# Performance work log

Hardware: AMD Instinct MI355X
Metric: run time of the kernel (lower is better)

The kernel has to match this reference:

```python
import jax, jax.numpy as jnp
import numpy as np

EPS = 1e-8  # numerical guard in padded (masked) softmax denominator


def setup_inputs() -> dict:
    key = jax.random.key(0)
    k1, k2 = jax.random.split(key)
    B, N, D = 8, 2048, 3
    coordinates = jax.random.normal(k1, (B, N, D), dtype=jnp.float32)
    masks = (jax.random.uniform(k2, (B, N, N)) < 0.9).astype(jnp.float32)
    sigma = jnp.ones((1,), dtype=jnp.float32)  # NonNeg learned scalar
    return {"coordinates": coordinates, "masks": masks, "sigma": sigma}


def reference(coordinates, masks, sigma):
    # pairwise squared euclidean distances: ||xi||^2 - 2 xi.xj + ||xj||^2
    norms = jnp.sum(coordinates ** 2, axis=-1, keepdims=True)            # [B,N,1]
    inner = jnp.einsum('bnd,bmd->bnm', coordinates, coordinates)         # [B,N,N]
    distances = norms - 2.0 * inner + jnp.swapaxes(norms, -1, -2)        # [B,N,N]
    # Gaussian kernel
    A = jnp.exp(-distances / (sigma ** 2))                               # [B,N,N]
    # padded_softmax: mask then row-normalize (A is positive, so this is a
    # masked softmax over -d/sigma^2 along the last axis)
    A = A * masks
    return A / (jnp.sum(A, axis=-1, keepdims=True) + EPS)
```

## Files before the change

### kernel.cpp

```cpp
#include <hip/hip_runtime.h>
#include <math.h>


#define NN      2048
#define THREADS 256
#define WPB     4
#define EPS     1e-8f

typedef float vfloat4 __attribute__((ext_vector_type(4)));

__global__ __launch_bounds__(THREADS) void gauss_adj_kernel(
    const float* __restrict__ coords,
    const float* __restrict__ masks,
    const float* __restrict__ sigma,
    float* __restrict__ out)
{
    const int row  = blockIdx.x * WPB + (threadIdx.x >> 6);
    const int lane = threadIdx.x & 63;
    const int b    = row >> 11;
    const int i    = row & (NN - 1);

    const float* cb = coords + (size_t)b * NN * 3;
    const float xi = cb[i * 3 + 0];
    const float yi = cb[i * 3 + 1];
    const float zi = cb[i * 3 + 2];
    const float s  = sigma[0];
    const float inv_s2 = 1.0f / (s * s);

    const vfloat4* mrow = (const vfloat4*)(masks + (size_t)row * NN);
    vfloat4*       orow = (vfloat4*)(out + (size_t)row * NN);
    const float4*  c4   = (const float4*)cb;

    vfloat4 a[8];
    float lsum = 0.0f;

    #pragma unroll
    for (int w = 0; w < 8; ++w) {
        const int q = w * 64 + lane;
        const vfloat4 m = __builtin_nontemporal_load(&mrow[q]);
        const float4 c0 = c4[3 * q + 0];
        const float4 c1 = c4[3 * q + 1];
        const float4 c2 = c4[3 * q + 2];

        float dx, dy, dz, d;
        dx = xi - c0.x; dy = yi - c0.y; dz = zi - c0.z;
        d  = dx * dx + dy * dy + dz * dz;
        const float a0 = __expf(-d * inv_s2) * m.x;

        dx = xi - c0.w; dy = yi - c1.x; dz = zi - c1.y;
        d  = dx * dx + dy * dy + dz * dz;
        const float a1 = __expf(-d * inv_s2) * m.y;

        dx = xi - c1.z; dy = yi - c1.w; dz = zi - c2.x;
        d  = dx * dx + dy * dy + dz * dz;
        const float a2 = __expf(-d * inv_s2) * m.z;

        dx = xi - c2.y; dy = yi - c2.z; dz = zi - c2.w;
        d  = dx * dx + dy * dy + dz * dz;
        const float a3 = __expf(-d * inv_s2) * m.w;

        vfloat4 av;
        av.x = a0; av.y = a1; av.z = a2; av.w = a3;
        a[w] = av;
        lsum += (a0 + a1) + (a2 + a3);
    }

    #pragma unroll
    for (int off = 32; off > 0; off >>= 1)
        lsum += __shfl_xor(lsum, off, 64);

    const float inv = 1.0f / (lsum + EPS);

    #pragma unroll
    for (int w = 0; w < 8; ++w) {
        const int q = w * 64 + lane;
        vfloat4 o = a[w];
        o.x *= inv; o.y *= inv; o.z *= inv; o.w *= inv;
        __builtin_nontemporal_store(o, &orow[q]);
    }
}

extern "C" void kernel_launch(void* const* d_in, const int* in_sizes, int n_in,
                              void* d_out, int out_size, void* d_ws, size_t ws_size,
                              hipStream_t stream) {
    const float* coords = (const float*)d_in[0];
    const float* masks  = (const float*)d_in[1];
    const float* sigma  = (const float*)d_in[2];
    float* out = (float*)d_out;

    const int B    = in_sizes[0] / (NN * 3);
    const int rows = B * NN;
    gauss_adj_kernel<<<rows / WPB, THREADS, 0, stream>>>(coords, masks, sigma, out);
}
```

Before: 237.2 us.

## Process four rows per wave with double-buffered mask loads and LDS coordinates

```diff
diff --git a/kernel.cpp b/kernel.cpp
--- a/kernel.cpp
+++ b/kernel.cpp
@@ -4,80 +4,94 @@
 
 #define NN      2048
 #define THREADS 256
-#define WPB     4
+#define RPW     4
+#define ROWS_PER_BLOCK 16
 #define EPS     1e-8f
 
-typedef float vfloat4 __attribute__((ext_vector_type(4)));
+typedef float vf4 __attribute__((ext_vector_type(4)));
 
-__global__ __launch_bounds__(THREADS) void gauss_adj_kernel(
+__global__ __launch_bounds__(THREADS, 4) void gauss_adj_kernel(
     const float* __restrict__ coords,
     const float* __restrict__ masks,
     const float* __restrict__ sigma,
     float* __restrict__ out)
 {
-    const int row  = blockIdx.x * WPB + (threadIdx.x >> 6);
-    const int lane = threadIdx.x & 63;
-    const int b    = row >> 11;
-    const int i    = row & (NN - 1);
+    const int tid  = threadIdx.x;
+    const int wid  = tid >> 6;
+    const int lane = tid & 63;
+    const int rowBase = blockIdx.x * ROWS_PER_BLOCK;
+    const int b = rowBase >> 11;
+
+    __shared__ __align__(16) float sx[NN];
+    __shared__ __align__(16) float sy[NN];
+    __shared__ __align__(16) float sz[NN];
 
     const float* cb = coords + (size_t)b * NN * 3;
-    const float xi = cb[i * 3 + 0];
-    const float yi = cb[i * 3 + 1];
-    const float zi = cb[i * 3 + 2];
-    const float s  = sigma[0];
-    const float inv_s2 = 1.0f / (s * s);
+    for (int idx = tid; idx < NN; idx += THREADS) {
+        sx[idx] = cb[idx * 3 + 0];
+        sy[idx] = cb[idx * 3 + 1];
+        sz[idx] = cb[idx * 3 + 2];
+    }
+    __syncthreads();
 
-    const vfloat4* mrow = (const vfloat4*)(masks + (size_t)row * NN);
-    vfloat4*       orow = (vfloat4*)(out + (size_t)row * NN);
-    const float4*  c4   = (const float4*)cb;
+    const float s = sigma[0];
+    const float cexp = -1.44269504088896341f / (s * s);
 
-    vfloat4 a[8];
-    float lsum = 0.0f;
+    const int r0 = rowBase + wid * RPW;
+    const vf4* sx4 = (const vf4*)sx;
+    const vf4* sy4 = (const vf4*)sy;
+    const vf4* sz4 = (const vf4*)sz;
 
-    #pragma unroll
-    for (int w = 0; w < 8; ++w) {
-        const int q = w * 64 + lane;
-        const vfloat4 m = __builtin_nontemporal_load(&mrow[q]);
-        const float4 c0 = c4[3 * q + 0];
-        const float4 c1 = c4[3 * q + 1];
-        const float4 c2 = c4[3 * q + 2];
+    vf4 A[8], B[8];
 
-        float dx, dy, dz, d;
-        dx = xi - c0.x; dy = yi - c0.y; dz = zi - c0.z;
-        d  = dx * dx + dy * dy + dz * dz;
-        const float a0 = __expf(-d * inv_s2) * m.x;
+#define LOADM(BUF, R) { \
+    const vf4* mrow_ = (const vf4*)(masks + (size_t)(r0 + (R)) * NN); \
+    _Pragma("unroll") \
+    for (int w = 0; w < 8; ++w) BUF[w] = mrow_[w * 64 + lane]; }
 
-        dx = xi - c0.w; dy = yi - c1.x; dz = zi - c1.y;
-        d  = dx * dx + dy * dy + dz * dz;
-        const float a1 = __expf(-d * inv_s2) * m.y;
+#define PROC(BUF, R) { \
+    const int i_ = (r0 + (R)) & (NN - 1); \
+    const float xi = sx[i_], yi = sy[i_], zi = sz[i_]; \
+    float lsum = 0.0f; \
+    _Pragma("unroll") \
+    for (int w = 0; w < 8; ++w) { \
+        const int q_ = w * 64 + lane; \
+        const vf4 X = sx4[q_], Y = sy4[q_], Z = sz4[q_]; \
+        vf4 v = BUF[w]; \
+        float dx, dy, dz, d; \
+        dx = xi - X.x; dy = yi - Y.x; dz = zi - Z.x; d = dx*dx + dy*dy + dz*dz; \
+        v.x *= exp2f(d * cexp); \
+        dx = xi - X.y; dy = yi - Y.y; dz = zi - Z.y; d = dx*dx + dy*dy + dz*dz; \
+        v.y *= exp2f(d * cexp); \
+        dx = xi - X.z; dy = yi - Y.z; dz = zi - Z.z; d = dx*dx + dy*dy + dz*dz; \
+        v.z *= exp2f(d * cexp); \
+        dx = xi - X.w; dy = yi - Y.w; dz = zi - Z.w; d = dx*dx + dy*dy + dz*dz; \
+        v.w *= exp2f(d * cexp); \
+        BUF[w] = v; \
+        lsum += (v.x + v.y) + (v.z + v.w); \
+    } \
+    _Pragma("unroll") \
+    for (int off = 32; off > 0; off >>= 1) lsum += __shfl_xor(lsum, off, 64); \
+    const float inv_ = 1.0f / (lsum + EPS); \
+    vf4* orow_ = (vf4*)(out + (size_t)(r0 + (R)) * NN); \
+    _Pragma("unroll") \
+    for (int w = 0; w < 8; ++w) { \
+        vf4 o = BUF[w]; \
+        o.x *= inv_; o.y *= inv_; o.z *= inv_; o.w *= inv_; \
+        __builtin_nontemporal_store(o, &orow_[w * 64 + lane]); \
+    } }
 
-        dx = xi - c1.z; dy = yi - c1.w; dz = zi - c2.x;
-        d  = dx * dx + dy * dy + dz * dz;
-        const float a2 = __expf(-d * inv_s2) * m.z;
+    LOADM(A, 0)
+    LOADM(B, 1)
+    PROC(A, 0)
+    LOADM(A, 2)
+    PROC(B, 1)
+    LOADM(B, 3)
+    PROC(A, 2)
+    PROC(B, 3)
 
-        dx = xi - c2.y; dy = yi - c2.z; dz = zi - c2.w;
-        d  = dx * dx + dy * dy + dz * dz;
-        const float a3 = __expf(-d * inv_s2) * m.w;
-
-        vfloat4 av;
-        av.x = a0; av.y = a1; av.z = a2; av.w = a3;
-        a[w] = av;
-        lsum += (a0 + a1) + (a2 + a3);
-    }
-
-    #pragma unroll
-    for (int off = 32; off > 0; off >>= 1)
-        lsum += __shfl_xor(lsum, off, 64);
-
-    const float inv = 1.0f / (lsum + EPS);
-
-    #pragma unroll
-    for (int w = 0; w < 8; ++w) {
-        const int q = w * 64 + lane;
-        vfloat4 o = a[w];
-        o.x *= inv; o.y *= inv; o.z *= inv; o.w *= inv;
-        __builtin_nontemporal_store(o, &orow[q]);
-    }
+#undef LOADM
+#undef PROC
 }
 
 extern "C" void kernel_launch(void* const* d_in, const int* in_sizes, int n_in,
@@ -90,5 +104,5 @@
 
     const int B    = in_sizes[0] / (NN * 3);
     const int rows = B * NN;
-    gauss_adj_kernel<<<rows / WPB, THREADS, 0, stream>>>(coords, masks, sigma, out);
+    gauss_adj_kernel<<<rows / ROWS_PER_BLOCK, THREADS, 0, stream>>>(coords, masks, sigma, out);
 }
```

Measured after the change: 247.5 us. 4.4% more time.

## Stage precomputed coordinate terms in LDS and split each row across 256 threads

Applied to the files above, without the earlier changes.

```diff
diff --git a/kernel.cpp b/kernel.cpp
--- a/kernel.cpp
+++ b/kernel.cpp
@@ -3,81 +3,88 @@
 
 
 #define NN      2048
-#define THREADS 256
-#define WPB     4
+#define THREADS 512
 #define EPS     1e-8f
 
-typedef float vfloat4 __attribute__((ext_vector_type(4)));
+typedef float vf4 __attribute__((ext_vector_type(4)));
 
-__global__ __launch_bounds__(THREADS) void gauss_adj_kernel(
+__global__ __launch_bounds__(THREADS, 8) void gauss_adj_kernel(
     const float* __restrict__ coords,
     const float* __restrict__ masks,
     const float* __restrict__ sigma,
     float* __restrict__ out)
 {
-    const int row  = blockIdx.x * WPB + (threadIdx.x >> 6);
-    const int lane = threadIdx.x & 63;
-    const int b    = row >> 11;
-    const int i    = row & (NN - 1);
+    const int tid = threadIdx.x;
+    const int rib = tid >> 8;
+    const int tir = tid & 255;
+    const int row = blockIdx.x * 2 + rib;
+    const int b   = row >> 11;
+    const int i   = row & (NN - 1);
 
+    __shared__ __align__(16) float qx[NN];
+    __shared__ __align__(16) float qy[NN];
+    __shared__ __align__(16) float qz[NN];
+    __shared__ __align__(16) float qw[NN];
+    __shared__ float red[8];
+
+    const float s = sigma[0];
+    const float C = 1.44269504088896341f / (s * s);
     const float* cb = coords + (size_t)b * NN * 3;
+
+    for (int idx = tid; idx < NN; idx += THREADS) {
+        const float x = cb[idx * 3 + 0];
+        const float y = cb[idx * 3 + 1];
+        const float z = cb[idx * 3 + 2];
+        qx[idx] = 2.0f * C * x;
+        qy[idx] = 2.0f * C * y;
+        qz[idx] = 2.0f * C * z;
+        qw[idx] = -C * (x * x + y * y + z * z);
+    }
+    __syncthreads();
+
     const float xi = cb[i * 3 + 0];
     const float yi = cb[i * 3 + 1];
     const float zi = cb[i * 3 + 2];
-    const float s  = sigma[0];
-    const float inv_s2 = 1.0f / (s * s);
 
-    const vfloat4* mrow = (const vfloat4*)(masks + (size_t)row * NN);
-    vfloat4*       orow = (vfloat4*)(out + (size_t)row * NN);
-    const float4*  c4   = (const float4*)cb;
+    const vf4* mrow = (const vf4*)(masks + (size_t)row * NN);
+    vf4*       orow = (vf4*)(out + (size_t)row * NN);
+    const vf4* qx4 = (const vf4*)qx;
+    const vf4* qy4 = (const vf4*)qy;
+    const vf4* qz4 = (const vf4*)qz;
+    const vf4* qw4 = (const vf4*)qw;
 
-    vfloat4 a[8];
+    vf4 m0 = mrow[tir];
+    vf4 m1 = mrow[256 + tir];
+
     float lsum = 0.0f;
 
-    #pragma unroll
-    for (int w = 0; w < 8; ++w) {
-        const int q = w * 64 + lane;
-        const vfloat4 m = __builtin_nontemporal_load(&mrow[q]);
-        const float4 c0 = c4[3 * q + 0];
-        const float4 c1 = c4[3 * q + 1];
-        const float4 c2 = c4[3 * q + 2];
+#define DOCHUNK(M, Q) { \
+        const int q_ = (Q); \
+        const vf4 X = qx4[q_], Y = qy4[q_], Z = qz4[q_], W = qw4[q_]; \
+        M.x *= exp2f(fmaf(xi, X.x, fmaf(yi, Y.x, fmaf(zi, Z.x, W.x)))); \
+        M.y *= exp2f(fmaf(xi, X.y, fmaf(yi, Y.y, fmaf(zi, Z.y, W.y)))); \
+        M.z *= exp2f(fmaf(xi, X.z, fmaf(yi, Y.z, fmaf(zi, Z.z, W.z)))); \
+        M.w *= exp2f(fmaf(xi, X.w, fmaf(yi, Y.w, fmaf(zi, Z.w, W.w)))); \
+        lsum += (M.x + M.y) + (M.z + M.w); \
+    }
 
-        float dx, dy, dz, d;
-        dx = xi - c0.x; dy = yi - c0.y; dz = zi - c0.z;
-        d  = dx * dx + dy * dy + dz * dz;
-        const float a0 = __expf(-d * inv_s2) * m.x;
-
-        dx = xi - c0.w; dy = yi - c1.x; dz = zi - c1.y;
-        d  = dx * dx + dy * dy + dz * dz;
-        const float a1 = __expf(-d * inv_s2) * m.y;
-
-        dx = xi - c1.z; dy = yi - c1.w; dz = zi - c2.x;
-        d  = dx * dx + dy * dy + dz * dz;
-        const float a2 = __expf(-d * inv_s2) * m.z;
-
-        dx = xi - c2.y; dy = yi - c2.z; dz = zi - c2.w;
-        d  = dx * dx + dy * dy + dz * dz;
-        const float a3 = __expf(-d * inv_s2) * m.w;
-
-        vfloat4 av;
-        av.x = a0; av.y = a1; av.z = a2; av.w = a3;
-        a[w] = av;
-        lsum += (a0 + a1) + (a2 + a3);
-    }
+    DOCHUNK(m0, tir)
+    DOCHUNK(m1, 256 + tir)
+#undef DOCHUNK
 
     #pragma unroll
     for (int off = 32; off > 0; off >>= 1)
         lsum += __shfl_xor(lsum, off, 64);
+    if ((tid & 63) == 0) red[tid >> 6] = lsum;
+    __syncthreads();
+    const int rb = rib * 4;
+    const float tot = (red[rb] + red[rb + 1]) + (red[rb + 2] + red[rb + 3]);
+    const float inv = 1.0f / (tot + EPS);
 
-    const float inv = 1.0f / (lsum + EPS);
-
-    #pragma unroll
-    for (int w = 0; w < 8; ++w) {
-        const int q = w * 64 + lane;
-        vfloat4 o = a[w];
-        o.x *= inv; o.y *= inv; o.z *= inv; o.w *= inv;
-        __builtin_nontemporal_store(o, &orow[q]);
-    }
+    m0.x *= inv; m0.y *= inv; m0.z *= inv; m0.w *= inv;
+    m1.x *= inv; m1.y *= inv; m1.z *= inv; m1.w *= inv;
+    __builtin_nontemporal_store(m0, &orow[tir]);
+    __builtin_nontemporal_store(m1, &orow[256 + tir]);
 }
 
 extern "C" void kernel_launch(void* const* d_in, const int* in_sizes, int n_in,
@@ -90,5 +97,5 @@
 
     const int B    = in_sizes[0] / (NN * 3);
     const int rows = B * NN;
-    gauss_adj_kernel<<<rows / WPB, THREADS, 0, stream>>>(coords, masks, sigma, out);
+    gauss_adj_kernel<<<rows / 2, THREADS, 0, stream>>>(coords, masks, sigma, out);
 }
```

Result: no change. 238.9 us (+0.7%).
